# Optimization experiments

Hardware: AMD Instinct MI355X
Metric: run time of the kernel (lower is better)

## Reference

```python
import jax, jax.numpy as jnp
import numpy as np

EPS = 1e-6  # VN-ReLU direction-norm epsilon
K_NN = 16


def vec_linear(x, W):
    # x: (B, Cin, 3, ...), W: (Cout, Cin) -> (B, Cout, 3, ...)
    return jnp.einsum('oi,bi...->bo...', W, x)


def vec_lna(x, W, U):
    # VecLinear + VN-LeakyReLU(negative_slope=0) acting on vector dim (axis 2)
    p = jnp.einsum('oi,bi...->bo...', W, x)   # feature map
    d = jnp.einsum('oi,bi...->bo...', U, x)   # direction map
    dot = jnp.sum(p * d, axis=2, keepdims=True)
    dsq = jnp.sum(d * d, axis=2, keepdims=True)
    return jnp.where(dot >= 0, p, p - (dot / (dsq + EPS)) * d)


def setup_inputs() -> dict:
    B, N = 2, 4096
    h, c, L = 128, 128, 4
    ks = jax.random.split(jax.random.key(0), 8)
    s = lambda k, shape, fan: (jax.random.normal(k, shape, jnp.float32) / np.sqrt(fan)).astype(jnp.float32)
    return {
        'x': jax.random.normal(ks[0], (B, 3, N), jnp.float32),
        'W_in': s(ks[1], (h, 3), 3),
        'U_in': s(ks[2], (h, 3), 3),
        'Wl': s(ks[3], (L, h, h), h),
        'Ul': s(ks[4], (L, h, h), h),
        'Wg': s(ks[5], (L, h, 2 * h), 2 * h),
        'Ug': s(ks[6], (L, h, 2 * h), 2 * h),
        'W_out': s(ks[7], (c, L * h), L * h),
    }


def reference(x, W_in, U_in, Wl, Ul, Wg, Ug, W_out):
    B, _, N = x.shape
    K = K_NN
    pts = jnp.transpose(x, (0, 2, 1))                      # (B, N, 3)
    # squared euclidean distance (same KNN ordering as torch.cdist p=2 + topk smallest)
    sq = jnp.sum(pts * pts, axis=-1)                       # (B, N)
    d2 = sq[:, :, None] + sq[:, None, :] - 2.0 * jnp.einsum('bnd,bmd->bnm', pts, pts)
    _, idx = jax.lax.top_k(-d2, K)                         # (B, N, K) nearest, sorted
    neighbors = jax.vmap(lambda p, i: p[i])(pts, idx)      # (B, N, K, 3) gather
    neighbors = jnp.transpose(neighbors, (0, 3, 1, 2))[:, None]  # (B, 1, 3, N, K)

    x4 = x[:, None]                                        # (B, 1, 3, N)
    x_pad = jnp.broadcast_to(x4[..., None], neighbors.shape)
    # F.normalize(x, dim=2) with eps=1e-12 clamp
    x_dir = x4 / jnp.maximum(jnp.linalg.norm(x4, axis=2, keepdims=True), 1e-12)
    cross = jnp.cross(jnp.broadcast_to(x_dir[..., None], neighbors.shape), neighbors, axis=2)
    y = jnp.concatenate([cross, neighbors - x_pad, x_pad], axis=1)  # (B, 3, 3, N, K)

    h_feat = vec_lna(y, W_in, U_in)                        # (B, h, 3, N, K)
    h_feat = jnp.mean(h_feat, axis=-1)                     # meanpool over K -> (B, h, 3, N)

    y = h_feat
    feats = []
    for i in range(Wl.shape[0]):
        y = vec_lna(y, Wl[i], Ul[i])                       # (B, h, 3, N)
        yg = jnp.mean(y, axis=-1, keepdims=True)
        y = jnp.concatenate([y, jnp.broadcast_to(yg, y.shape)], axis=1)  # (B, 2h, 3, N)
        y = vec_lna(y, Wg[i], Ug[i])                       # (B, h, 3, N)
        feats.append(y)

    out = vec_linear(jnp.concatenate(feats, axis=1), W_out)  # (B, c, 3, N)
    return (jnp.mean(out, axis=-1), out)
```

## Files before the change

kernel.cpp:

```cpp
#include <hip/hip_runtime.h>
#include <hip/hip_bf16.h>
#include <cfloat>


typedef __attribute__((ext_vector_type(8))) short short8;
typedef __attribute__((ext_vector_type(4))) float f32x4;

__device__ __forceinline__ unsigned short f2bf(float f) {
    union { float f; unsigned u; } v; v.f = f;
    unsigned r = v.u + 0x7fffu + ((v.u >> 16) & 1u);
    return (unsigned short)(r >> 16);
}
__device__ __forceinline__ float bf2f(unsigned short h) {
    union { unsigned u; float f; } v; v.u = ((unsigned)h) << 16;
    return v.f;
}

__global__ __launch_bounds__(256) void setup_kernel(const float* __restrict__ x,
                                                    float4* __restrict__ pts4,
                                                    const float* __restrict__ Wl,
                                                    const float* __restrict__ Ul,
                                                    const float* __restrict__ Wg,
                                                    const float* __restrict__ Ug,
                                                    const float* __restrict__ Wout,
                                                    unsigned short* __restrict__ Ah,
                                                    unsigned short* __restrict__ Al,
                                                    int N, int B) {
    int t = blockIdx.x * 256 + threadIdx.x;
    if (t < B * N) {
        int b = t / N, n = t - b * N;
        const float* xb = x + (long)b * 3 * N;
        float px = xb[n], py = xb[N + n], pz = xb[2 * N + n];
        pts4[t] = make_float4(px, py, pz, px * px + py * py + pz * pz);
    }
    int g, r, M; long base;
    if (t < 262144) { g = t >> 15; r = t & 32767; M = 256; base = (long)g << 15; }
    else { int t2 = t - 262144; g = 8 + (t2 >> 14); r = t2 & 16383; M = 128;
           base = 262144 + (long)(g - 8) * 16384; }
    int MF = M >> 4;
    int ks = r / (MF * 512);
    int mf = (r >> 9) % MF;
    int lane = (r >> 3) & 63;
    int j = r & 7;
    int m = mf * 16 + (lane & 15);
    int k = ks * 32 + ((lane >> 4) << 3) + j;
    const float* src; int ldw; int row;
    if (g < 4) {
        ldw = 128; row = m & 127;
        src = (m < 128) ? (Wl + (long)g * 128 * 128) : (Ul + (long)g * 128 * 128);
    } else if (g < 8) {
        ldw = 256; row = m & 127;
        int l = g - 4;
        src = (m < 128) ? (Wg + (long)l * 128 * 256) : (Ug + (long)l * 128 * 256);
    } else {
        ldw = 512; row = m;
        src = Wout + (g - 8) * 128;
    }
    float v = src[(long)row * ldw + k];
    unsigned short h = f2bf(v);
    Ah[base + r] = h;
    Al[base + r] = f2bf(v - bf2f(h));
}

__global__ __launch_bounds__(1024) void knn_kernel(const float4* __restrict__ pts4,
                                                   int* __restrict__ idxOut, int N) {
    __shared__ float4 cbuf[4096];
    int t = threadIdx.x;
    int tilesPerB = N / 16;
    int b = blockIdx.x / tilesPerB;
    int q = (blockIdx.x % tilesPerB) * 16 + (t >> 6);
    int lane = t & 63;

    for (int i = t; i < N; i += 1024) cbuf[i] = pts4[b * N + i];
    __syncthreads();

    float4 Q = cbuf[q];
    unsigned ku; int ki;

    {
        float4 C = cbuf[lane];
        float dot = Q.x * C.x + Q.y * C.y + Q.z * C.z;
        float d2 = Q.w + C.w - 2.0f * dot;
        unsigned u = __float_as_uint(d2);
        u ^= (unsigned)((int)u >> 31) | 0x80000000u;
        double key = (double)u * 4096.0 + (double)lane;
#pragma unroll
        for (int k = 2; k <= 64; k <<= 1) {
#pragma unroll
            for (int j = k >> 1; j > 0; j >>= 1) {
                double other = __shfl_xor(key, j);
                bool takeMin = (((lane & j) == 0) == ((lane & k) == 0));
                double mn = fmin(key, other), mx = fmax(key, other);
                key = takeMin ? mn : mx;
            }
        }
        long long kl = (long long)key;
        ki = (int)(kl & 4095);
        ku = (unsigned)(kl >> 12);
    }
    unsigned Tu = (unsigned)__builtin_amdgcn_readlane((int)ku, 15);

    for (int c0 = 64; c0 < N; c0 += 64) {
        float4 C = cbuf[c0 + lane];
        float dot = Q.x * C.x + Q.y * C.y + Q.z * C.z;
        float d2 = Q.w + C.w - 2.0f * dot;
        unsigned u = __float_as_uint(d2);
        u ^= (unsigned)((int)u >> 31) | 0x80000000u;
        int ci = c0 + lane;
        unsigned long long mask = __ballot(u <= Tu);
        while (mask) {
            int src = __ffsll(mask) - 1;
            mask &= mask - 1;
            unsigned vu = (unsigned)__builtin_amdgcn_readlane((int)u, src);
            int      vi = __builtin_amdgcn_readlane(ci, src);
            unsigned kum1 = (unsigned)__builtin_amdgcn_update_dpp(
                                (int)ku, (int)ku, 0x111, 0xF, 0xF, false);
            int      kim1 = __builtin_amdgcn_update_dpp(
                                ki, ki, 0x111, 0xF, 0xF, false);
            if (lane == 0) { kum1 = 0u; kim1 = (-2147483647 - 1); }
            bool lem1 = (vu < kum1) || (vu == kum1 && vi < kim1);
            bool ltj  = (vu < ku)   || (vu == ku   && vi < ki);
            unsigned knu = lem1 ? kum1 : (ltj ? vu : ku);
            int      kni = lem1 ? kim1 : (ltj ? vi : ki);
            if (lane < 16) { ku = knu; ki = kni; }
        }
        Tu = (unsigned)__builtin_amdgcn_readlane((int)ku, 15);
    }
    if (lane < 16) idxOut[(b * N + q) * 16 + lane] = ki;
}

__global__ __launch_bounds__(1024) void edgegemm0_kernel(
    const float4* __restrict__ pts4, const int* __restrict__ idx,
    const float* __restrict__ Win, const float* __restrict__ Uin,
    const unsigned short* __restrict__ Aph, const unsigned short* __restrict__ Apl,
    unsigned short* __restrict__ Oh, unsigned short* __restrict__ Ol,
    float* __restrict__ part, int N)
{
    __shared__ float4 nbuf[32][16];
    __shared__ float4 cpt[32];
    __shared__ unsigned short flds[2][3][2][2048];
    int t = threadIdx.x;
    int lane = t & 63, w = t >> 6;
    int ng = w >> 3, wv = w & 7;
    int b = blockIdx.x >> 7;
    int tile = blockIdx.x & 127;
    int n0 = tile * 32;

    if (t < 512) {
        int pl = t >> 4, k = t & 15;
        int nb = idx[(b * N + n0 + pl) * 16 + k];
        nbuf[pl][k] = pts4[b * N + nb];
    } else if (t < 544) {
        cpt[t - 512] = pts4[b * N + n0 + (t - 512)];
    }
    __syncthreads();
    {
        int o = t & 127, grp = t >> 7;
        float w0 = Win[o * 3], w1 = Win[o * 3 + 1], w2 = Win[o * 3 + 2];
        float u0 = Uin[o * 3], u1 = Uin[o * 3 + 1], u2 = Uin[o * 3 + 2];
        for (int pl = grp * 4; pl < grp * 4 + 4; ++pl) {
            float4 c4 = cpt[pl];
            float inv = 1.0f / fmaxf(sqrtf(c4.w), 1e-12f);
            float ax = c4.x * inv, ay = c4.y * inv, az = c4.z * inv;
            float a0 = 0.f, a1 = 0.f, a2 = 0.f;
            for (int k = 0; k < 16; ++k) {
                float4 nb = nbuf[pl][k];
                float cr0 = ay * nb.z - az * nb.y;
                float cr1 = az * nb.x - ax * nb.z;
                float cr2 = ax * nb.y - ay * nb.x;
                float df0 = nb.x - c4.x, df1 = nb.y - c4.y, df2 = nb.z - c4.z;
                float P0 = w0 * cr0 + w1 * df0 + w2 * c4.x;
                float P1 = w0 * cr1 + w1 * df1 + w2 * c4.y;
                float P2 = w0 * cr2 + w1 * df2 + w2 * c4.z;
                float D0 = u0 * cr0 + u1 * df0 + u2 * c4.x;
                float D1 = u0 * cr1 + u1 * df1 + u2 * c4.y;
                float D2 = u0 * cr2 + u1 * df2 + u2 * c4.z;
                float dot = P0 * D0 + P1 * D1 + P2 * D2;
                float dsq = D0 * D0 + D1 * D1 + D2 * D2;
                if (dot < 0.0f) {
                    float s = dot / (dsq + 1e-6f);
                    P0 -= s * D0; P1 -= s * D1; P2 -= s * D2;
                }
                a0 += P0; a1 += P1; a2 += P2;
            }
            float vals[3] = { a0 * (1.0f / 16.0f), a1 * (1.0f / 16.0f), a2 * (1.0f / 16.0f) };
            int ngg = pl >> 4, col = pl & 15;
            int li = ((o >> 3) << 7) + (col << 3) + (o & 7);
#pragma unroll
            for (int c = 0; c < 3; ++c) {
                unsigned short hh = f2bf(vals[c]);
                flds[ngg][c][0][li] = hh;
                flds[ngg][c][1][li] = f2bf(vals[c] - bf2f(hh));
            }
        }
    }
    __syncthreads();

    int ncol = tile * 32 + ng * 16 + (lane & 15);
    f32x4 accP[3] = {};
    f32x4 accD[3] = {};
#pragma unroll
    for (int ks = 0; ks < 4; ++ks) {
        short8 bh[3], bl[3];
        int li = (((ks << 2) + (lane >> 4)) << 7) + ((lane & 15) << 3);
#pragma unroll
        for (int c = 0; c < 3; ++c) {
            bh[c] = *(const short8*)&flds[ng][c][0][li];
            bl[c] = *(const short8*)&flds[ng][c][1][li];
        }
        long aoffP = (((long)ks * 16 + wv) * 64 + lane) * 8;
        short8 ahP = *(const short8*)(Aph + aoffP);
        short8 alP = *(const short8*)(Apl + aoffP);
#pragma unroll
        for (int c = 0; c < 3; ++c) {
            accP[c] = __builtin_amdgcn_mfma_f32_16x16x32_bf16(ahP, bh[c], accP[c], 0, 0, 0);
            accP[c] = __builtin_amdgcn_mfma_f32_16x16x32_bf16(ahP, bl[c], accP[c], 0, 0, 0);
            accP[c] = __builtin_amdgcn_mfma_f32_16x16x32_bf16(alP, bh[c], accP[c], 0, 0, 0);
        }
        long aoffD = (((long)ks * 16 + 8 + wv) * 64 + lane) * 8;
        short8 ahD = *(const short8*)(Aph + aoffD);
        short8 alD = *(const short8*)(Apl + aoffD);
#pragma unroll
        for (int c = 0; c < 3; ++c) {
            accD[c] = __builtin_amdgcn_mfma_f32_16x16x32_bf16(ahD, bh[c], accD[c], 0, 0, 0);
            accD[c] = __builtin_amdgcn_mfma_f32_16x16x32_bf16(ahD, bl[c], accD[c], 0, 0, 0);
            accD[c] = __builtin_amdgcn_mfma_f32_16x16x32_bf16(alD, bh[c], accD[c], 0, 0, 0);
        }
    }

    int obase = 16 * wv + ((lane >> 4) << 2);
    float Pv[3][4];
#pragma unroll
    for (int r = 0; r < 4; ++r) {
        float P[3], D[3];
#pragma unroll
        for (int c = 0; c < 3; ++c) { P[c] = accP[c][r]; D[c] = accD[c][r]; }
        float dot = P[0] * D[0] + P[1] * D[1] + P[2] * D[2];
        float dsq = D[0] * D[0] + D[1] * D[1] + D[2] * D[2];
        if (dot < 0.0f) {
            float s = dot / (dsq + 1e-6f);
            P[0] -= s * D[0]; P[1] -= s * D[1]; P[2] -= s * D[2];
        }
        Pv[0][r] = P[0]; Pv[1][r] = P[1]; Pv[2][r] = P[2];
    }
#pragma unroll
    for (int c = 0; c < 3; ++c) {
        unsigned short hs[4], ls[4];
#pragma unroll
        for (int r = 0; r < 4; ++r) {
            hs[r] = f2bf(Pv[c][r]);
            ls[r] = f2bf(Pv[c][r] - bf2f(hs[r]));
        }
        long ooff = ((long)(b * 3 + c) * N + ncol) * 128 + obase;
        *(ushort4*)(Oh + ooff) = make_ushort4(hs[0], hs[1], hs[2], hs[3]);
        *(ushort4*)(Ol + ooff) = make_ushort4(ls[0], ls[1], ls[2], ls[3]);
#pragma unroll
        for (int r = 0; r < 4; ++r) {
            float v = Pv[c][r];
            v += __shfl_xor(v, 1);
            v += __shfl_xor(v, 2);
            v += __shfl_xor(v, 4);
            v += __shfl_xor(v, 8);
            if ((lane & 15) == 0)
                part[((long)(b * 3 + c) * 256 + tile * 2 + ng) * 128 + (obase + r)] = v;
        }
    }
}

template<bool HASNEXT>
__global__ __launch_bounds__(1024) void fused_kernel(
    const unsigned short* __restrict__ Aph, const unsigned short* __restrict__ Apl,
    long aOffG, long aOffOut, long aOffNext,
    unsigned short* __restrict__ y1h, unsigned short* __restrict__ y1l,
    const float* __restrict__ biasP, const float* __restrict__ biasD,
    float* __restrict__ Ofp, float* __restrict__ part, int accum)
{
    const int N = 4096;
    __shared__ unsigned short ylds[2][3][2][2048];
    int t = threadIdx.x;
    int lane = t & 63, w = t >> 6;
    int ng = w >> 3, wv = w & 7;
    int b = blockIdx.x >> 7;
    int tile = blockIdx.x & 127;
    int ncol = tile * 32 + ng * 16 + (lane & 15);
    int kq = (lane >> 4) << 3;

    {
        f32x4 accP[3] = {};
        f32x4 accD[3] = {};
        const unsigned short* AhB = Aph + aOffG;
        const unsigned short* AlB = Apl + aOffG;
#pragma unroll
        for (int ks = 0; ks < 4; ++ks) {
            short8 bh[3], bl[3];
#pragma unroll
            for (int c = 0; c < 3; ++c) {
                long boff = ((long)(b * 3 + c) * N + ncol) * 128 + ks * 32 + kq;
                bh[c] = *(const short8*)(y1h + boff);
                bl[c] = *(const short8*)(y1l + boff);
            }
            long aoffP = (((long)ks * 16 + wv) * 64 + lane) * 8;
            short8 ahP = *(const short8*)(AhB + aoffP);
            short8 alP = *(const short8*)(AlB + aoffP);
#pragma unroll
            for (int c = 0; c < 3; ++c) {
                accP[c] = __builtin_amdgcn_mfma_f32_16x16x32_bf16(ahP, bh[c], accP[c], 0, 0, 0);
                accP[c] = __builtin_amdgcn_mfma_f32_16x16x32_bf16(ahP, bl[c], accP[c], 0, 0, 0);
                accP[c] = __builtin_amdgcn_mfma_f32_16x16x32_bf16(alP, bh[c], accP[c], 0, 0, 0);
            }
            long aoffD = (((long)ks * 16 + 8 + wv) * 64 + lane) * 8;
            short8 ahD = *(const short8*)(AhB + aoffD);
            short8 alD = *(const short8*)(AlB + aoffD);
#pragma unroll
            for (int c = 0; c < 3; ++c) {
                accD[c] = __builtin_amdgcn_mfma_f32_16x16x32_bf16(ahD, bh[c], accD[c], 0, 0, 0);
                accD[c] = __builtin_amdgcn_mfma_f32_16x16x32_bf16(ahD, bl[c], accD[c], 0, 0, 0);
                accD[c] = __builtin_amdgcn_mfma_f32_16x16x32_bf16(alD, bh[c], accD[c], 0, 0, 0);
            }
        }
        int obase = 16 * wv + ((lane >> 4) << 2);
        float Pv[3][4];
#pragma unroll
        for (int r = 0; r < 4; ++r) {
            int o = obase + r;
            float P[3], D[3];
#pragma unroll
            for (int c = 0; c < 3; ++c) {
                long bb = ((long)(b * 128 + o)) * 3 + c;
                P[c] = accP[c][r] + biasP[bb];
                D[c] = accD[c][r] + biasD[bb];
            }
            float dot = P[0] * D[0] + P[1] * D[1] + P[2] * D[2];
            float dsq = D[0] * D[0] + D[1] * D[1] + D[2] * D[2];
            if (dot < 0.0f) {
                float s = dot / (dsq + 1e-6f);
                P[0] -= s * D[0]; P[1] -= s * D[1]; P[2] -= s * D[2];
            }
            Pv[0][r] = P[0]; Pv[1][r] = P[1]; Pv[2][r] = P[2];
        }
#pragma unroll
        for (int c = 0; c < 3; ++c) {
            unsigned short hs[4], ls[4];
#pragma unroll
            for (int r = 0; r < 4; ++r) {
                hs[r] = f2bf(Pv[c][r]);
                ls[r] = f2bf(Pv[c][r] - bf2f(hs[r]));
            }
            int li = ((obase >> 3) << 7) + ((lane & 15) << 3) + (obase & 7);
            *(ushort4*)&ylds[ng][c][0][li] = make_ushort4(hs[0], hs[1], hs[2], hs[3]);
            *(ushort4*)&ylds[ng][c][1][li] = make_ushort4(ls[0], ls[1], ls[2], ls[3]);
        }
    }
    __syncthreads();

    {
        f32x4 accO[3] = {};
        const unsigned short* AoH = Aph + aOffOut;
        const unsigned short* AoL = Apl + aOffOut;
#pragma unroll
        for (int ks = 0; ks < 4; ++ks) {
            short8 yh[3], yl[3];
            int li = (((ks << 2) + (lane >> 4)) << 7) + ((lane & 15) << 3);
#pragma unroll
            for (int c = 0; c < 3; ++c) {
                yh[c] = *(const short8*)&ylds[ng][c][0][li];
                yl[c] = *(const short8*)&ylds[ng][c][1][li];
            }
            long aoff = (((long)ks * 8 + wv) * 64 + lane) * 8;
            short8 ah = *(const short8*)(AoH + aoff);
            short8 al = *(const short8*)(AoL + aoff);
#pragma unroll
            for (int c = 0; c < 3; ++c) {
                accO[c] = __builtin_amdgcn_mfma_f32_16x16x32_bf16(ah, yh[c], accO[c], 0, 0, 0);
                accO[c] = __builtin_amdgcn_mfma_f32_16x16x32_bf16(ah, yl[c], accO[c], 0, 0, 0);
                accO[c] = __builtin_amdgcn_mfma_f32_16x16x32_bf16(al, yh[c], accO[c], 0, 0, 0);
            }
        }
        int obase = 16 * wv + ((lane >> 4) << 2);
        float Ov[3][4];
#pragma unroll
        for (int r = 0; r < 4; ++r) {
            int o = obase + r;
#pragma unroll
            for (int c = 0; c < 3; ++c) {
                long off = ((long)(b * 128 + o) * 3 + c) * N + ncol;
                float v = accO[c][r];
                if (accum) v += Ofp[off];
                Ofp[off] = v;
                Ov[c][r] = v;
            }
        }
        if (!HASNEXT) {
#pragma unroll
            for (int c = 0; c < 3; ++c) {
#pragma unroll
                for (int r = 0; r < 4; ++r) {
                    float v = Ov[c][r];
                    v += __shfl_xor(v, 1);
                    v += __shfl_xor(v, 2);
                    v += __shfl_xor(v, 4);
                    v += __shfl_xor(v, 8);
                    if ((lane & 15) == 0)
                        part[((long)(b * 3 + c) * 256 + tile * 2 + ng) * 128 + (obase + r)] = v;
                }
            }
        }
    }

    if (HASNEXT) {
        f32x4 accP[3] = {};
        f32x4 accD[3] = {};
        const unsigned short* AnH = Aph + aOffNext;
        const unsigned short* AnL = Apl + aOffNext;
#pragma unroll
        for (int ks = 0; ks < 4; ++ks) {
            short8 bh[3], bl[3];
            int li = (((ks << 2) + (lane >> 4)) << 7) + ((lane & 15) << 3);
#pragma unroll
            for (int c = 0; c < 3; ++c) {
                bh[c] = *(const short8*)&ylds[ng][c][0][li];
                bl[c] = *(const short8*)&ylds[ng][c][1][li];
            }
            long aoffP = (((long)ks * 16 + wv) * 64 + lane) * 8;
            short8 ahP = *(const short8*)(AnH + aoffP);
            short8 alP = *(const short8*)(AnL + aoffP);
#pragma unroll
            for (int c = 0; c < 3; ++c) {
                accP[c] = __builtin_amdgcn_mfma_f32_16x16x32_bf16(ahP, bh[c], accP[c], 0, 0, 0);
                accP[c] = __builtin_amdgcn_mfma_f32_16x16x32_bf16(ahP, bl[c], accP[c], 0, 0, 0);
                accP[c] = __builtin_amdgcn_mfma_f32_16x16x32_bf16(alP, bh[c], accP[c], 0, 0, 0);
            }
            long aoffD = (((long)ks * 16 + 8 + wv) * 64 + lane) * 8;
            short8 ahD = *(const short8*)(AnH + aoffD);
            short8 alD = *(const short8*)(AnL + aoffD);
#pragma unroll
            for (int c = 0; c < 3; ++c) {
                accD[c] = __builtin_amdgcn_mfma_f32_16x16x32_bf16(ahD, bh[c], accD[c], 0, 0, 0);
                accD[c] = __builtin_amdgcn_mfma_f32_16x16x32_bf16(ahD, bl[c], accD[c], 0, 0, 0);
                accD[c] = __builtin_amdgcn_mfma_f32_16x16x32_bf16(alD, bh[c], accD[c], 0, 0, 0);
            }
        }
        int obase = 16 * wv + ((lane >> 4) << 2);
        float Pv[3][4];
#pragma unroll
        for (int r = 0; r < 4; ++r) {
            float P[3], D[3];
#pragma unroll
            for (int c = 0; c < 3; ++c) { P[c] = accP[c][r]; D[c] = accD[c][r]; }
            float dot = P[0] * D[0] + P[1] * D[1] + P[2] * D[2];
            float dsq = D[0] * D[0] + D[1] * D[1] + D[2] * D[2];
            if (dot < 0.0f) {
                float s = dot / (dsq + 1e-6f);
                P[0] -= s * D[0]; P[1] -= s * D[1]; P[2] -= s * D[2];
            }
            Pv[0][r] = P[0]; Pv[1][r] = P[1]; Pv[2][r] = P[2];
        }
#pragma unroll
        for (int c = 0; c < 3; ++c) {
            unsigned short hs[4], ls[4];
#pragma unroll
            for (int r = 0; r < 4; ++r) {
                hs[r] = f2bf(Pv[c][r]);
                ls[r] = f2bf(Pv[c][r] - bf2f(hs[r]));
            }
            long ooff = ((long)(b * 3 + c) * N + ncol) * 128 + obase;
            *(ushort4*)(y1h + ooff) = make_ushort4(hs[0], hs[1], hs[2], hs[3]);
            *(ushort4*)(y1l + ooff) = make_ushort4(ls[0], ls[1], ls[2], ls[3]);
#pragma unroll
            for (int r = 0; r < 4; ++r) {
                float v = Pv[c][r];
                v += __shfl_xor(v, 1);
                v += __shfl_xor(v, 2);
                v += __shfl_xor(v, 4);
                v += __shfl_xor(v, 8);
                if ((lane & 15) == 0)
                    part[((long)(b * 3 + c) * 256 + tile * 2 + ng) * 128 + (obase + r)] = v;
            }
        }
    }
}

__global__ __launch_bounds__(1024) void ygredbias_kernel(const float* __restrict__ part,
                                                         const float* __restrict__ Wg,
                                                         const float* __restrict__ Ug,
                                                         float* __restrict__ biasP,
                                                         float* __restrict__ biasD) {
    __shared__ float red[8][128];
    __shared__ float ygs[128];
    int bc = blockIdx.x;
    int t = threadIdx.x;
    int o = t & 127, g = t >> 7;
    float s = 0.f;
    for (int seg = g * 32; seg < g * 32 + 32; ++seg)
        s += part[((long)bc * 256 + seg) * 128 + o];
    red[g][o] = s;
    __syncthreads();
    if (t < 128) {
        float r = 0.f;
#pragma unroll
        for (int k = 0; k < 8; ++k) r += red[k][t];
        ygs[t] = r * (1.0f / 4096.0f);
    }
    __syncthreads();
    if (t < 256) {
        int oo = t & 127; bool isD = t >= 128;
        const float* row = (isD ? Ug : Wg) + oo * 256 + 128;
        float s2 = 0.f;
        for (int i = 0; i < 128; ++i) s2 = fmaf(row[i], ygs[i], s2);
        int b = bc / 3, c = bc % 3;
        (isD ? biasD : biasP)[((long)(b * 128 + oo)) * 3 + c] = s2;
    }
}

__global__ __launch_bounds__(1024) void out0red_kernel(const float* __restrict__ part,
                                                       float* __restrict__ out0) {
    __shared__ float red[8][128];
    int bc = blockIdx.x;
    int t = threadIdx.x;
    int o = t & 127, g = t >> 7;
    float s = 0.f;
    for (int seg = g * 32; seg < g * 32 + 32; ++seg)
        s += part[((long)bc * 256 + seg) * 128 + o];
    red[g][o] = s;
    __syncthreads();
    if (t < 128) {
        float r = 0.f;
#pragma unroll
        for (int k = 0; k < 8; ++k) r += red[k][t];
        int b = bc / 3, c = bc % 3;
        out0[((long)(b * 128) + t) * 3 + c] = r * (1.0f / 4096.0f);
    }
}

extern "C" void kernel_launch(void* const* d_in, const int* in_sizes, int n_in,
                              void* d_out, int out_size, void* d_ws, size_t ws_size,
                              hipStream_t stream) {
    const float* x    = (const float*)d_in[0];
    const float* Win  = (const float*)d_in[1];
    const float* Uin  = (const float*)d_in[2];
    const float* Wl   = (const float*)d_in[3];
    const float* Ul   = (const float*)d_in[4];
    const float* Wg   = (const float*)d_in[5];
    const float* Ug   = (const float*)d_in[6];
    const float* Wout = (const float*)d_in[7];

    const int B = 2, N = 4096, H = 128;
    float* out0 = (float*)d_out;
    float* out1 = out0 + (long)B * H * 3;

    float* ws = (float*)d_ws;
    long off = 0;
    float4* pts4 = (float4*)ws;                  off += (long)B * N * 4;
    int* idx = (int*)(ws + off);                 off += (long)B * N * 16;
    const long ACT = (long)B * 3 * N * H;
    unsigned short* y1h = (unsigned short*)(ws + off);  off += ACT / 2;
    unsigned short* y1l = (unsigned short*)(ws + off);  off += ACT / 2;
    unsigned short* Aph = (unsigned short*)(ws + off);  off += 327680 / 2;
    unsigned short* Apl = (unsigned short*)(ws + off);  off += 327680 / 2;
    float* part  = ws + off;                     off += 6L * 256 * 128;
    float* biasP = ws + off;                     off += B * H * 3;
    float* biasD = ws + off;                     off += B * H * 3;

    setup_kernel<<<1280, 256, 0, stream>>>(x, pts4, Wl, Ul, Wg, Ug, Wout, Aph, Apl, N, B);
    knn_kernel<<<B * (N / 16), 1024, 0, stream>>>(pts4, idx, N);

    edgegemm0_kernel<<<256, 1024, 0, stream>>>(pts4, idx, Win, Uin,
                                               Aph, Apl, y1h, y1l, part, N);

    for (int l = 0; l < 4; ++l) {
        ygredbias_kernel<<<6, 1024, 0, stream>>>(part,
            Wg + (long)l * H * 256, Ug + (long)l * H * 256, biasP, biasD);
        long aG = (long)(4 + l) * 32768;
        long aO = 262144 + (long)l * 16384;
        if (l < 3) {
            fused_kernel<true><<<256, 1024, 0, stream>>>(
                Aph, Apl, aG, aO, (long)(l + 1) * 32768,
                y1h, y1l, biasP, biasD, out1, part, l > 0 ? 1 : 0);
        } else {
            fused_kernel<false><<<256, 1024, 0, stream>>>(
                Aph, Apl, aG, aO, 0L,
                y1h, y1l, biasP, biasD, out1, part, 1);
        }
    }
    out0red_kernel<<<6, 1024, 0, stream>>>(part, out0);
}
```

Baseline: 231.3 us.

## Fold bias and output reductions into producer kernels via last-block election

Removes the separate ygredbias and out0red launches by having the last block of each edge/fused kernel (picked by an atomic counter and threadfence) reduce the partial sums and compute the next layer's global bias, or out0 at the end. Bias buffers are double-buffered, so the next layer reads what the previous kernel's tail wrote. The KNN loop also now reads the threshold only when some candidate passed. This cuts five small launches and their gaps, but the reduction now runs serially in a single block at the tail of each kernel and adds a grid-wide atomic.

```diff
diff --git a/kernel.cpp b/kernel.cpp
--- a/kernel.cpp
+++ b/kernel.cpp
@@ -25,8 +25,10 @@
                                                     const float* __restrict__ Wout,
                                                     unsigned short* __restrict__ Ah,
                                                     unsigned short* __restrict__ Al,
+                                                    int* __restrict__ cnt,
                                                     int N, int B) {
     int t = blockIdx.x * 256 + threadIdx.x;
+    if (t < 8) cnt[t] = 0;
     if (t < B * N) {
         int b = t / N, n = t - b * N;
         const float* xb = x + (long)b * 3 * N;
@@ -108,25 +110,90 @@
         u ^= (unsigned)((int)u >> 31) | 0x80000000u;
         int ci = c0 + lane;
         unsigned long long mask = __ballot(u <= Tu);
-        while (mask) {
-            int src = __ffsll(mask) - 1;
-            mask &= mask - 1;
-            unsigned vu = (unsigned)__builtin_amdgcn_readlane((int)u, src);
-            int      vi = __builtin_amdgcn_readlane(ci, src);
-            unsigned kum1 = (unsigned)__builtin_amdgcn_update_dpp(
-                                (int)ku, (int)ku, 0x111, 0xF, 0xF, false);
-            int      kim1 = __builtin_amdgcn_update_dpp(
-                                ki, ki, 0x111, 0xF, 0xF, false);
-            if (lane == 0) { kum1 = 0u; kim1 = (-2147483647 - 1); }
-            bool lem1 = (vu < kum1) || (vu == kum1 && vi < kim1);
-            bool ltj  = (vu < ku)   || (vu == ku   && vi < ki);
-            unsigned knu = lem1 ? kum1 : (ltj ? vu : ku);
-            int      kni = lem1 ? kim1 : (ltj ? vi : ki);
-            if (lane < 16) { ku = knu; ki = kni; }
-        }
-        Tu = (unsigned)__builtin_amdgcn_readlane((int)ku, 15);
+        if (mask) {
+            do {
+                int src = __ffsll(mask) - 1;
+                mask &= mask - 1;
+                unsigned vu = (unsigned)__builtin_amdgcn_readlane((int)u, src);
+                int      vi = __builtin_amdgcn_readlane(ci, src);
+                unsigned kum1 = (unsigned)__builtin_amdgcn_update_dpp(
+                                    (int)ku, (int)ku, 0x111, 0xF, 0xF, false);
+                int      kim1 = __builtin_amdgcn_update_dpp(
+                                    ki, ki, 0x111, 0xF, 0xF, false);
+                if (lane == 0) { kum1 = 0u; kim1 = (-2147483647 - 1); }
+                bool lem1 = (vu < kum1) || (vu == kum1 && vi < kim1);
+                bool ltj  = (vu < ku)   || (vu == ku   && vi < ki);
+                unsigned knu = lem1 ? kum1 : (ltj ? vu : ku);
+                int      kni = lem1 ? kim1 : (ltj ? vi : ki);
+                if (lane < 16) { ku = knu; ki = kni; }
+            } while (mask);
+            Tu = (unsigned)__builtin_amdgcn_readlane((int)ku, 15);
+        }
     }
     if (lane < 16) idxOut[(b * N + q) * 16 + lane] = ki;
+}
+
+__device__ __forceinline__ void tail_bias_reduce(const float* __restrict__ part,
+                                                 const float* __restrict__ WgN,
+                                                 const float* __restrict__ UgN,
+                                                 float* __restrict__ bP,
+                                                 float* __restrict__ bD,
+                                                 int t, float (*red)[128], float (*ygs)[128]) {
+    int o = t & 127, g = (t >> 7) & 7;
+    for (int bc = 0; bc < 6; ++bc) {
+        float s = 0.f;
+        const float* p = part + ((long)bc * 256 + g * 32) * 128 + o;
+        for (int seg = 0; seg < 32; ++seg) s += p[(long)seg * 128];
+        red[g][o] = s;
+        __syncthreads();
+        if (t < 128) {
+            float r = 0.f;
+#pragma unroll
+            for (int k2 = 0; k2 < 8; ++k2) r += red[k2][t];
+            ygs[bc][t] = r * (1.0f / 4096.0f);
+        }
+        __syncthreads();
+    }
+    for (int j = t; j < 1536; j += 1024) {
+        bool isD = j >= 768;
+        int idx2 = isD ? j - 768 : j;
+        int c = idx2 % 3; int oo = (idx2 / 3) % 128; int bb = idx2 / 384;
+        const float* row = (isD ? UgN : WgN) + oo * 256 + 128;
+        const float* y = &ygs[bb * 3 + c][0];
+        float s2 = 0.f;
+        for (int i = 0; i < 128; ++i) s2 = fmaf(row[i], y[i], s2);
+        (isD ? bD : bP)[idx2] = s2;
+    }
+}
+
+__device__ __forceinline__ void tail_out0_reduce(const float* __restrict__ part,
+                                                 float* __restrict__ out0,
+                                                 int t, float (*red)[128]) {
+    int o = t & 127, g = (t >> 7) & 7;
+    for (int bc = 0; bc < 6; ++bc) {
+        float s = 0.f;
+        const float* p = part + ((long)bc * 256 + g * 32) * 128 + o;
+        for (int seg = 0; seg < 32; ++seg) s += p[(long)seg * 128];
+        red[g][o] = s;
+        __syncthreads();
+        if (t < 128) {
+            float r = 0.f;
+#pragma unroll
+            for (int k2 = 0; k2 < 8; ++k2) r += red[k2][t];
+            out0[((long)((bc / 3) * 128) + t) * 3 + (bc % 3)] = r * (1.0f / 4096.0f);
+        }
+        __syncthreads();
+    }
+}
+
+__device__ __forceinline__ bool elect_last(int* cnt, int nblocks, int* lastFlag) {
+    __threadfence();
+    __syncthreads();
+    if (threadIdx.x == 0) *lastFlag = (atomicAdd(cnt, 1) == nblocks - 1) ? 1 : 0;
+    __syncthreads();
+    bool last = (*lastFlag != 0);
+    if (last) __threadfence();
+    return last;
 }
 
 __global__ __launch_bounds__(1024) void edgegemm0_kernel(
@@ -134,11 +201,17 @@
     const float* __restrict__ Win, const float* __restrict__ Uin,
     const unsigned short* __restrict__ Aph, const unsigned short* __restrict__ Apl,
     unsigned short* __restrict__ Oh, unsigned short* __restrict__ Ol,
-    float* __restrict__ part, int N)
+    float* __restrict__ part,
+    const float* __restrict__ Wg0, const float* __restrict__ Ug0,
+    float* __restrict__ bP0, float* __restrict__ bD0,
+    int* __restrict__ cnt, int N)
 {
     __shared__ float4 nbuf[32][16];
     __shared__ float4 cpt[32];
     __shared__ unsigned short flds[2][3][2][2048];
+    __shared__ float red[8][128];
+    __shared__ float ygs[6][128];
+    __shared__ int lastFlag;
     int t = threadIdx.x;
     int lane = t & 63, w = t >> 6;
     int ng = w >> 3, wv = w & 7;
@@ -265,6 +338,9 @@
                 part[((long)(b * 3 + c) * 256 + tile * 2 + ng) * 128 + (obase + r)] = v;
         }
     }
+
+    if (elect_last(cnt, 256, &lastFlag))
+        tail_bias_reduce(part, Wg0, Ug0, bP0, bD0, t, red, ygs);
 }
 
 template<bool HASNEXT>
@@ -273,10 +349,17 @@
     long aOffG, long aOffOut, long aOffNext,
     unsigned short* __restrict__ y1h, unsigned short* __restrict__ y1l,
     const float* __restrict__ biasP, const float* __restrict__ biasD,
-    float* __restrict__ Ofp, float* __restrict__ part, int accum)
+    const float* __restrict__ WgN, const float* __restrict__ UgN,
+    float* __restrict__ bPOut, float* __restrict__ bDOut,
+    float* __restrict__ out0,
+    float* __restrict__ Ofp, float* __restrict__ part,
+    int* __restrict__ cnt, int accum)
 {
     const int N = 4096;
     __shared__ unsigned short ylds[2][3][2][2048];
+    __shared__ float red[8][128];
+    __shared__ float ygs[6][128];
+    __shared__ int lastFlag;
     int t = threadIdx.x;
     int lane = t & 63, w = t >> 6;
     int ng = w >> 3, wv = w & 7;
@@ -478,57 +561,10 @@
             }
         }
     }
-}
-
-__global__ __launch_bounds__(1024) void ygredbias_kernel(const float* __restrict__ part,
-                                                         const float* __restrict__ Wg,
-                                                         const float* __restrict__ Ug,
-                                                         float* __restrict__ biasP,
-                                                         float* __restrict__ biasD) {
-    __shared__ float red[8][128];
-    __shared__ float ygs[128];
-    int bc = blockIdx.x;
-    int t = threadIdx.x;
-    int o = t & 127, g = t >> 7;
-    float s = 0.f;
-    for (int seg = g * 32; seg < g * 32 + 32; ++seg)
-        s += part[((long)bc * 256 + seg) * 128 + o];
-    red[g][o] = s;
-    __syncthreads();
-    if (t < 128) {
-        float r = 0.f;
-#pragma unroll
-        for (int k = 0; k < 8; ++k) r += red[k][t];
-        ygs[t] = r * (1.0f / 4096.0f);
-    }
-    __syncthreads();
-    if (t < 256) {
-        int oo = t & 127; bool isD = t >= 128;
-        const float* row = (isD ? Ug : Wg) + oo * 256 + 128;
-        float s2 = 0.f;
-        for (int i = 0; i < 128; ++i) s2 = fmaf(row[i], ygs[i], s2);
-        int b = bc / 3, c = bc % 3;
-        (isD ? biasD : biasP)[((long)(b * 128 + oo)) * 3 + c] = s2;
-    }
-}
-
-__global__ __launch_bounds__(1024) void out0red_kernel(const float* __restrict__ part,
-                                                       float* __restrict__ out0) {
-    __shared__ float red[8][128];
-    int bc = blockIdx.x;
-    int t = threadIdx.x;
-    int o = t & 127, g = t >> 7;
-    float s = 0.f;
-    for (int seg = g * 32; seg < g * 32 + 32; ++seg)
-        s += part[((long)bc * 256 + seg) * 128 + o];
-    red[g][o] = s;
-    __syncthreads();
-    if (t < 128) {
-        float r = 0.f;
-#pragma unroll
-        for (int k = 0; k < 8; ++k) r += red[k][t];
-        int b = bc / 3, c = bc % 3;
-        out0[((long)(b * 128) + t) * 3 + c] = r * (1.0f / 4096.0f);
+
+    if (elect_last(cnt, 256, &lastFlag)) {
+        if (HASNEXT) tail_bias_reduce(part, WgN, UgN, bPOut, bDOut, t, red, ygs);
+        else         tail_out0_reduce(part, out0, t, red);
     }
 }
 
@@ -558,29 +594,38 @@
     unsigned short* Aph = (unsigned short*)(ws + off);  off += 327680 / 2;
     unsigned short* Apl = (unsigned short*)(ws + off);  off += 327680 / 2;
     float* part  = ws + off;                     off += 6L * 256 * 128;
-    float* biasP = ws + off;                     off += B * H * 3;
-    float* biasD = ws + off;                     off += B * H * 3;
-
-    setup_kernel<<<1280, 256, 0, stream>>>(x, pts4, Wl, Ul, Wg, Ug, Wout, Aph, Apl, N, B);
+    float* biasA = ws + off;                     off += 2L * 768;
+    float* biasB = ws + off;                     off += 2L * 768;
+    int* cnt     = (int*)(ws + off);             off += 8;
+
+    setup_kernel<<<1280, 256, 0, stream>>>(x, pts4, Wl, Ul, Wg, Ug, Wout,
+                                           Aph, Apl, cnt, N, B);
     knn_kernel<<<B * (N / 16), 1024, 0, stream>>>(pts4, idx, N);
 
     edgegemm0_kernel<<<256, 1024, 0, stream>>>(pts4, idx, Win, Uin,
-                                               Aph, Apl, y1h, y1l, part, N);
-
+                                               Aph, Apl, y1h, y1l, part,
+                                               Wg, Ug, biasA, biasA + 768,
+                                               &cnt[0], N);
+
+    float* bIn = biasA;
+    float* bOut = biasB;
     for (int l = 0; l < 4; ++l) {
-        ygredbias_kernel<<<6, 1024, 0, stream>>>(part,
-            Wg + (long)l * H * 256, Ug + (long)l * H * 256, biasP, biasD);
         long aG = (long)(4 + l) * 32768;
         long aO = 262144 + (long)l * 16384;
         if (l < 3) {
             fused_kernel<true><<<256, 1024, 0, stream>>>(
                 Aph, Apl, aG, aO, (long)(l + 1) * 32768,
-                y1h, y1l, biasP, biasD, out1, part, l > 0 ? 1 : 0);
+                y1h, y1l, bIn, bIn + 768,
+                Wg + (long)(l + 1) * H * 256, Ug + (long)(l + 1) * H * 256,
+                bOut, bOut + 768, nullptr,
+                out1, part, &cnt[1 + l], l > 0 ? 1 : 0);
         } else {
             fused_kernel<false><<<256, 1024, 0, stream>>>(
                 Aph, Apl, aG, aO, 0L,
-                y1h, y1l, biasP, biasD, out1, part, 1);
-        }
-    }
-    out0red_kernel<<<6, 1024, 0, stream>>>(part, out0);
-}
+                y1h, y1l, bIn, bIn + 768,
+                nullptr, nullptr, nullptr, nullptr, out0,
+                out1, part, &cnt[1 + l], 1);
+        }
+        float* tmp = bIn; bIn = bOut; bOut = tmp;
+    }
+}
```

New measurement: 825.6 us. +257.0%, slower.
